# Kernel tuning notes

Hardware: AMD Instinct MI355X
Metric: run time of the kernel (lower is better)

## Reference

```python
import jax, jax.numpy as jnp
import numpy as np

STEP_SIZE = 0.01
ITERATION = 1.0
F_FORCING = 8.0
N_STEPS = int(round(ITERATION / STEP_SIZE))  # 100 fixed RK4 steps

BATCH = 8192
INPUT_SIZE = 784
SYSTEM_COUNT = 1024
OUTPUT_SIZE = 10


def setup_inputs() -> dict:
    key = jax.random.key(0)
    k_x, k_w1, k_b1, k_w2, k_b2 = jax.random.split(key, 5)
    x = jax.random.normal(k_x, (BATCH, INPUT_SIZE), dtype=jnp.float32)
    # nn.Linear-style params (out_features, in_features)
    s1 = 1.0 / np.sqrt(INPUT_SIZE)
    W1 = jax.random.uniform(k_w1, (SYSTEM_COUNT, INPUT_SIZE), jnp.float32, -s1, s1)
    b1 = jax.random.uniform(k_b1, (SYSTEM_COUNT,), jnp.float32, -s1, s1)
    s2 = 1.0 / np.sqrt(SYSTEM_COUNT)
    W2 = jax.random.uniform(k_w2, (OUTPUT_SIZE, SYSTEM_COUNT), jnp.float32, -s2, s2)
    b2 = jax.random.uniform(k_b2, (OUTPUT_SIZE,), jnp.float32, -s2, s2)
    return {"x": x, "W1": W1, "b1": b1, "W2": W2, "b2": b2}


def _lorenz96(x):
    # (roll(x,-1) - roll(x,2)) * roll(x,1) - x + F   along feature dim 1
    return (jnp.roll(x, -1, axis=1) - jnp.roll(x, 2, axis=1)) * jnp.roll(x, 1, axis=1) - x + F_FORCING


def _rk4_integrate(x0):
    h = jnp.float32(STEP_SIZE)

    def step(x, _):
        k1 = _lorenz96(x)
        k2 = _lorenz96(x + 0.5 * h * k1)
        k3 = _lorenz96(x + 0.5 * h * k2)
        k4 = _lorenz96(x + h * k3)
        x_next = x + (h / 6.0) * (k1 + 2.0 * k2 + 2.0 * k3 + k4)
        return x_next, None

    xT, _ = jax.lax.scan(step, x0, None, length=N_STEPS)
    return xT


def reference(x, W1, b1, W2, b2):
    h = x @ W1.T + b1                 # [B, systemCount]
    h = _rk4_integrate(h)             # RK4 over [0, iteration], step 0.01
    logits = h @ W2.T + b2            # [B, output_size]
    return jax.nn.log_softmax(logits, axis=1)
```

## Files before the change

kernel.cpp:

```cpp
#include <hip/hip_runtime.h>
#include <hip/hip_bf16.h>
#include <math.h>

#define BATCH 8192
#define INSZ 784
#define SYS 1024
#define OUTSZ 10
#define NSTEP 100
#define HSTEP 0.01f
#define FFORCE 8.0f

typedef short short8 __attribute__((ext_vector_type(8)));
typedef float float4v __attribute__((ext_vector_type(4)));
typedef float v2f __attribute__((ext_vector_type(2)));

static __device__ __forceinline__ short f2bf(float x) {
    __hip_bfloat16 b = __float2bfloat16(x);
    return __builtin_bit_cast(short, b);
}
static __device__ __forceinline__ float bf2f(short s) {
    unsigned int u = ((unsigned int)(unsigned short)s) << 16;
    return __builtin_bit_cast(float, u);
}

static __device__ __forceinline__ v2f pkfma(v2f a, v2f b, v2f c) {
    return __builtin_elementwise_fma(a, b, c);
}
static __device__ __forceinline__ v2f mk2(float x, float y) {
    v2f r; r.x = x; r.y = y; return r;
}
static __device__ __forceinline__ v2f sh2(v2f v, int ln) {
    v2f r; r.x = __shfl(v.x, ln); r.y = __shfl(v.y, ln); return r;
}

#define BM2 64
#define BN2 64
#define BK2 32
#define LDK2 40

__global__ __launch_bounds__(256, 4) void gemm1_kernel(
    const float* __restrict__ x, const float* __restrict__ W1,
    const float* __restrict__ b1, float* __restrict__ h)
{
    __shared__ short Ah[BM2 * LDK2], Al[BM2 * LDK2];
    __shared__ short Bh[BN2 * LDK2], Bl[BN2 * LDK2];

    const int t  = threadIdx.x;
    const int bm = blockIdx.y * BM2;
    const int bn = blockIdx.x * BN2;

    const int srow = t >> 2;
    const int kq   = (t & 3) * 8;

    const int wv   = t >> 6;
    const int lane = t & 63;
    const int lm   = lane & 15;
    const int q    = lane >> 4;

    float4v acc[4];
    #pragma unroll
    for (int j = 0; j < 4; ++j) {
        acc[j][0] = 0.f; acc[j][1] = 0.f; acc[j][2] = 0.f; acc[j][3] = 0.f;
    }

    const float* xa0 = x  + (size_t)(bm + srow) * INSZ + kq;
    const float* wb0 = W1 + (size_t)(bn + srow) * INSZ + kq;

    for (int it = 0; it < 25; ++it) {
        const int k0 = it * BK2;
        {
            const bool valid = (k0 + kq) < INSZ;
            float va[8], vb[8];
            if (valid) {
                #pragma unroll
                for (int p = 0; p < 2; ++p) {
                    float4 xv = ((const float4*)(xa0 + k0))[p];
                    float4 bv = ((const float4*)(wb0 + k0))[p];
                    va[4*p+0] = xv.x; va[4*p+1] = xv.y; va[4*p+2] = xv.z; va[4*p+3] = xv.w;
                    vb[4*p+0] = bv.x; vb[4*p+1] = bv.y; vb[4*p+2] = bv.z; vb[4*p+3] = bv.w;
                }
            } else {
                #pragma unroll
                for (int j = 0; j < 8; ++j) { va[j] = 0.f; vb[j] = 0.f; }
            }
            short8 ahi, alo, bhi, blo;
            #pragma unroll
            for (int j = 0; j < 8; ++j) {
                short h1 = f2bf(va[j]);
                short l1 = f2bf(va[j] - bf2f(h1));
                short h2 = f2bf(vb[j]);
                short l2 = f2bf(vb[j] - bf2f(h2));
                ahi[j] = h1;  alo[j] = l1;
                bhi[j] = h2;  blo[j] = l2;
            }
            const int base = srow * LDK2 + kq;
            *(short8*)&Ah[base] = ahi;
            *(short8*)&Al[base] = alo;
            *(short8*)&Bh[base] = bhi;
            *(short8*)&Bl[base] = blo;
        }
        __syncthreads();

        const int aoff = (wv * 16 + lm) * LDK2 + q * 8;
        short8 ah = *(const short8*)&Ah[aoff];
        short8 al = *(const short8*)&Al[aoff];
        #pragma unroll
        for (int fj = 0; fj < 4; ++fj) {
            const int boff = (fj * 16 + lm) * LDK2 + q * 8;
            short8 bh = *(const short8*)&Bh[boff];
            short8 bl = *(const short8*)&Bl[boff];
            acc[fj] = __builtin_amdgcn_mfma_f32_16x16x32_bf16(ah, bh, acc[fj], 0, 0, 0);
            acc[fj] = __builtin_amdgcn_mfma_f32_16x16x32_bf16(ah, bl, acc[fj], 0, 0, 0);
            acc[fj] = __builtin_amdgcn_mfma_f32_16x16x32_bf16(al, bh, acc[fj], 0, 0, 0);
        }
        __syncthreads();
    }

    #pragma unroll
    for (int fj = 0; fj < 4; ++fj) {
        const int col  = bn + fj * 16 + lm;
        const float bias = b1[col];
        const int row0 = bm + wv * 16 + q * 4;
        #pragma unroll
        for (int r = 0; r < 4; ++r)
            h[(size_t)(row0 + r) * SYS + col] = acc[fj][r] + bias;
    }
}

__global__ __launch_bounds__(256, 4) void rk4_kernel(
    const float* __restrict__ hbuf, const float* __restrict__ W2,
    const float* __restrict__ b2, float* __restrict__ out)
{
    const int lane = threadIdx.x & 63;
    const int w    = threadIdx.x >> 6;
    const int rowA = blockIdx.x * 8 + w * 2;
    const int rowB = rowA + 1;

    const int laneL = (lane + 63) & 63;
    const int laneR = (lane + 1) & 63;

    v2f X[16];
    {
        const float4* a4 = (const float4*)(hbuf + (size_t)rowA * SYS) + lane * 4;
        const float4* b4 = (const float4*)(hbuf + (size_t)rowB * SYS) + lane * 4;
        #pragma unroll
        for (int k = 0; k < 4; ++k) {
            float4 av = a4[k], bv = b4[k];
            X[4*k+0] = mk2(av.x, bv.x);
            X[4*k+1] = mk2(av.y, bv.y);
            X[4*k+2] = mk2(av.z, bv.z);
            X[4*k+3] = mk2(av.w, bv.w);
        }
    }

    const v2f Fv     = mk2(FFORCE, FFORCE);
    const v2f c_half = mk2(0.5f * HSTEP, 0.5f * HSTEP);
    const v2f c_full = mk2(HSTEP, HSTEP);
    const v2f c_two  = mk2(2.0f, 2.0f);
    const v2f c_six  = mk2(HSTEP / 6.0f, HSTEP / 6.0f);

    v2f acc[16], T[16];

    auto deriv_ip = [&](v2f (&y)[16], v2f r1, v2f l1, v2f l2) {
        v2f y0o = y[0], y1o = y[1], y2o = y[2];
        v2f d0 = Fv - y[0], d1 = Fv - y[1], d15 = Fv - y[15];
        v2f p2 = y0o, p1 = y1o, cur = y[2];
        #pragma unroll
        for (int i = 2; i < 15; ++i) {
            v2f yp1 = (i < 14) ? y[i + 1] : y[15];
            v2f nv  = pkfma(yp1 - p2, p1, Fv - cur);
            p2 = p1; p1 = cur;
            if (i < 14) cur = y[i + 1];
            y[i] = nv;
        }
        y[15] = pkfma(r1 - p2, p1, d15);
        y[1]  = pkfma(y2o - l1, y0o, d1);
        y[0]  = pkfma(y1o - l2, l1, d0);
    };

    v2f r1x = sh2(X[0],  laneR);
    v2f l1x = sh2(X[15], laneL);
    v2f l2x = sh2(X[14], laneL);

    #pragma unroll 1
    for (int s = 0; s < NSTEP; ++s) {
        #pragma unroll
        for (int i = 2; i < 15; ++i)
            acc[i] = pkfma(X[i + 1] - X[i - 2], X[i - 1], Fv - X[i]);
        acc[15] = pkfma(r1x - X[13], X[14], Fv - X[15]);
        acc[1]  = pkfma(X[2] - l1x, X[0],  Fv - X[1]);
        acc[0]  = pkfma(X[1] - l2x, l1x,   Fv - X[0]);

        T[14] = pkfma(c_half, acc[14], X[14]);
        T[15] = pkfma(c_half, acc[15], X[15]);
        T[0]  = pkfma(c_half, acc[0],  X[0]);
        v2f r1 = sh2(T[0],  laneR);
        v2f l1 = sh2(T[15], laneL);
        v2f l2 = sh2(T[14], laneL);
        #pragma unroll
        for (int i = 1; i < 14; ++i) T[i] = pkfma(c_half, acc[i], X[i]);
        deriv_ip(T, r1, l1, l2);

        {
            v2f a;
            a = T[14]; acc[14] = pkfma(c_two, a, acc[14]); T[14] = pkfma(c_half, a, X[14]);
            a = T[15]; acc[15] = pkfma(c_two, a, acc[15]); T[15] = pkfma(c_half, a, X[15]);
            a = T[0];  acc[0]  = pkfma(c_two, a, acc[0]);  T[0]  = pkfma(c_half, a, X[0]);
            r1 = sh2(T[0],  laneR);
            l1 = sh2(T[15], laneL);
            l2 = sh2(T[14], laneL);
            #pragma unroll
            for (int i = 1; i < 14; ++i) {
                a = T[i]; acc[i] = pkfma(c_two, a, acc[i]); T[i] = pkfma(c_half, a, X[i]);
            }
        }
        deriv_ip(T, r1, l1, l2);

        {
            v2f a;
            a = T[14]; acc[14] = pkfma(c_two, a, acc[14]); T[14] = pkfma(c_full, a, X[14]);
            a = T[15]; acc[15] = pkfma(c_two, a, acc[15]); T[15] = pkfma(c_full, a, X[15]);
            a = T[0];  acc[0]  = pkfma(c_two, a, acc[0]);  T[0]  = pkfma(c_full, a, X[0]);
            r1 = sh2(T[0],  laneR);
            l1 = sh2(T[15], laneL);
            l2 = sh2(T[14], laneL);
            #pragma unroll
            for (int i = 1; i < 14; ++i) {
                a = T[i]; acc[i] = pkfma(c_two, a, acc[i]); T[i] = pkfma(c_full, a, X[i]);
            }
        }
        deriv_ip(T, r1, l1, l2);

        X[14] = pkfma(c_six, acc[14] + T[14], X[14]);
        X[15] = pkfma(c_six, acc[15] + T[15], X[15]);
        X[0]  = pkfma(c_six, acc[0]  + T[0],  X[0]);
        r1x = sh2(X[0],  laneR);
        l1x = sh2(X[15], laneL);
        l2x = sh2(X[14], laneL);
        #pragma unroll
        for (int i = 1; i < 14; ++i)
            X[i] = pkfma(c_six, acc[i] + T[i], X[i]);
    }

    v2f l[OUTSZ];
    #pragma unroll
    for (int o = 0; o < OUTSZ; ++o) {
        const float4* w4 = (const float4*)(W2 + (size_t)o * SYS) + lane * 4;
        v2f s2 = mk2(0.f, 0.f);
        #pragma unroll
        for (int k = 0; k < 4; ++k) {
            float4 wv = w4[k];
            s2 = pkfma(X[4*k+0], mk2(wv.x, wv.x), s2);
            s2 = pkfma(X[4*k+1], mk2(wv.y, wv.y), s2);
            s2 = pkfma(X[4*k+2], mk2(wv.z, wv.z), s2);
            s2 = pkfma(X[4*k+3], mk2(wv.w, wv.w), s2);
        }
        #pragma unroll
        for (int dlt = 1; dlt < 64; dlt <<= 1) {
            s2.x += __shfl_xor(s2.x, dlt);
            s2.y += __shfl_xor(s2.y, dlt);
        }
        const float bo = b2[o];
        l[o] = s2 + mk2(bo, bo);
    }

    v2f m = l[0];
    #pragma unroll
    for (int o = 1; o < OUTSZ; ++o) m = __builtin_elementwise_max(m, l[o]);
    v2f ssum = mk2(0.f, 0.f);
    #pragma unroll
    for (int o = 0; o < OUTSZ; ++o) {
        v2f d = l[o] - m;
        ssum = ssum + mk2(__expf(d.x), __expf(d.y));
    }
    const v2f lse = m + mk2(__logf(ssum.x), __logf(ssum.y));

    float vA = l[0].x - lse.x;
    float vB = l[0].y - lse.y;
    #pragma unroll
    for (int o = 1; o < OUTSZ; ++o) {
        if (lane == o) { vA = l[o].x - lse.x; vB = l[o].y - lse.y; }
    }
    if (lane < OUTSZ) {
        out[(size_t)rowA * OUTSZ + lane] = vA;
        out[(size_t)rowB * OUTSZ + lane] = vB;
    }
}

extern "C" void kernel_launch(void* const* d_in, const int* in_sizes, int n_in,
                              void* d_out, int out_size, void* d_ws, size_t ws_size,
                              hipStream_t stream)
{
    const float* x  = (const float*)d_in[0];
    const float* W1 = (const float*)d_in[1];
    const float* b1 = (const float*)d_in[2];
    const float* W2 = (const float*)d_in[3];
    const float* b2 = (const float*)d_in[4];
    float* out = (float*)d_out;
    float* h   = (float*)d_ws;

    dim3 g1(SYS / BN2, BATCH / BM2);
    gemm1_kernel<<<g1, 256, 0, stream>>>(x, W1, b1, h);

    rk4_kernel<<<BATCH / 8, 256, 0, stream>>>(h, W2, b2, out);
}
```

Baseline: 416.6 us.

## Pre-split x and W1 into bf16 hi/lo buffers before GEMM1

Adds a conversion kernel that splits x and W1 once into padded bf16 high and low parts stored in workspace. A new GEMM kernel then loads the pre-split shorts directly instead of converting fp32 to bf16 pairs inside every tile, which removes the repeated conversions from the inner loop. The split buffers add an extra launch plus write and read traffic. The new path only runs when the workspace is large enough, otherwise the old kernel is used.

After: 430.0 us. 1.03x slower.

```diff
diff --git a/kernel.cpp b/kernel.cpp
--- a/kernel.cpp
+++ b/kernel.cpp
@@ -9,6 +9,7 @@
 #define NSTEP 100
 #define HSTEP 0.01f
 #define FFORCE 8.0f
+#define KP 800
 
 typedef short short8 __attribute__((ext_vector_type(8)));
 typedef float float4v __attribute__((ext_vector_type(4)));
@@ -31,12 +32,150 @@
 }
 static __device__ __forceinline__ v2f sh2(v2f v, int ln) {
     v2f r; r.x = __shfl(v.x, ln); r.y = __shfl(v.y, ln); return r;
+}
+
+__global__ __launch_bounds__(256) void convert_kernel(
+    const float* __restrict__ x, const float* __restrict__ W1,
+    short* __restrict__ xh, short* __restrict__ xl,
+    short* __restrict__ wh, short* __restrict__ wl)
+{
+    const int total = (BATCH + SYS) * (KP / 8);
+    for (int idx = blockIdx.x * blockDim.x + threadIdx.x; idx < total;
+         idx += gridDim.x * blockDim.x) {
+        const int row = idx / (KP / 8);
+        const int ck  = idx - row * (KP / 8);
+
+        short8 hi, lo;
+        if (ck < INSZ / 8) {
+            const float* src = (row < BATCH)
+                ? (x + (size_t)row * INSZ)
+                : (W1 + (size_t)(row - BATCH) * INSZ);
+            float4 v0 = ((const float4*)src)[ck * 2];
+            float4 v1 = ((const float4*)src)[ck * 2 + 1];
+            float vv[8] = {v0.x, v0.y, v0.z, v0.w, v1.x, v1.y, v1.z, v1.w};
+            #pragma unroll
+            for (int j = 0; j < 8; ++j) {
+                short hj = f2bf(vv[j]);
+                hi[j] = hj;
+                lo[j] = f2bf(vv[j] - bf2f(hj));
+            }
+        } else {
+            #pragma unroll
+            for (int j = 0; j < 8; ++j) { hi[j] = 0; lo[j] = 0; }
+        }
+
+        short* dh; short* dl;
+        if (row < BATCH) {
+            dh = xh + (size_t)row * KP;
+            dl = xl + (size_t)row * KP;
+        } else {
+            dh = wh + (size_t)(row - BATCH) * KP;
+            dl = wl + (size_t)(row - BATCH) * KP;
+        }
+        *(short8*)(dh + ck * 8) = hi;
+        *(short8*)(dl + ck * 8) = lo;
+    }
 }
 
 #define BM2 64
 #define BN2 64
 #define BK2 32
 #define LDK2 40
+
+__global__ __launch_bounds__(256, 4) void gemm1s_kernel(
+    const short* __restrict__ xh, const short* __restrict__ xl,
+    const short* __restrict__ wh, const short* __restrict__ wl,
+    const float* __restrict__ b1, float* __restrict__ h)
+{
+    __shared__ short Ah[BM2 * LDK2], Al[BM2 * LDK2];
+    __shared__ short Bh[BN2 * LDK2], Bl[BN2 * LDK2];
+
+    const int t  = threadIdx.x;
+    const int bm = blockIdx.y * BM2;
+    const int bn = blockIdx.x * BN2;
+
+    const int srow = t >> 2;
+    const int kq   = (t & 3) * 8;
+
+    const int wv   = t >> 6;
+    const int wr   = wv >> 1;
+    const int wc   = wv & 1;
+    const int lane = t & 63;
+    const int lm   = lane & 15;
+    const int q    = lane >> 4;
+
+    float4v acc[2][2];
+    #pragma unroll
+    for (int mi = 0; mi < 2; ++mi)
+        #pragma unroll
+        for (int nj = 0; nj < 2; ++nj) {
+            acc[mi][nj][0] = 0.f; acc[mi][nj][1] = 0.f;
+            acc[mi][nj][2] = 0.f; acc[mi][nj][3] = 0.f;
+        }
+
+    const short* pxh = xh + (size_t)(bm + srow) * KP + kq;
+    const short* pxl = xl + (size_t)(bm + srow) * KP + kq;
+    const short* pwh = wh + (size_t)(bn + srow) * KP + kq;
+    const short* pwl = wl + (size_t)(bn + srow) * KP + kq;
+    const int sbase = srow * LDK2 + kq;
+
+    short8 ra = *(const short8*)(pxh);
+    short8 rb = *(const short8*)(pxl);
+    short8 rc = *(const short8*)(pwh);
+    short8 rd = *(const short8*)(pwl);
+
+    for (int it = 0; it < 25; ++it) {
+        *(short8*)&Ah[sbase] = ra;
+        *(short8*)&Al[sbase] = rb;
+        *(short8*)&Bh[sbase] = rc;
+        *(short8*)&Bl[sbase] = rd;
+        __syncthreads();
+
+        if (it < 24) {
+            const int k1 = (it + 1) * BK2;
+            ra = *(const short8*)(pxh + k1);
+            rb = *(const short8*)(pxl + k1);
+            rc = *(const short8*)(pwh + k1);
+            rd = *(const short8*)(pwl + k1);
+        }
+
+        short8 fah[2], fal[2], fbh[2], fbl[2];
+        #pragma unroll
+        for (int mi = 0; mi < 2; ++mi) {
+            const int ao = (wr * 32 + mi * 16 + lm) * LDK2 + q * 8;
+            fah[mi] = *(const short8*)&Ah[ao];
+            fal[mi] = *(const short8*)&Al[ao];
+        }
+        #pragma unroll
+        for (int nj = 0; nj < 2; ++nj) {
+            const int bo = (wc * 32 + nj * 16 + lm) * LDK2 + q * 8;
+            fbh[nj] = *(const short8*)&Bh[bo];
+            fbl[nj] = *(const short8*)&Bl[bo];
+        }
+        #pragma unroll
+        for (int mi = 0; mi < 2; ++mi)
+            #pragma unroll
+            for (int nj = 0; nj < 2; ++nj) {
+                acc[mi][nj] = __builtin_amdgcn_mfma_f32_16x16x32_bf16(fah[mi], fbh[nj], acc[mi][nj], 0, 0, 0);
+                acc[mi][nj] = __builtin_amdgcn_mfma_f32_16x16x32_bf16(fah[mi], fbl[nj], acc[mi][nj], 0, 0, 0);
+                acc[mi][nj] = __builtin_amdgcn_mfma_f32_16x16x32_bf16(fal[mi], fbh[nj], acc[mi][nj], 0, 0, 0);
+            }
+        __syncthreads();
+    }
+
+    #pragma unroll
+    for (int mi = 0; mi < 2; ++mi) {
+        const int row0 = bm + wr * 32 + mi * 16 + q * 4;
+        #pragma unroll
+        for (int nj = 0; nj < 2; ++nj) {
+            const int col  = bn + wc * 32 + nj * 16 + lm;
+            const float bias = b1[col];
+            #pragma unroll
+            for (int r = 0; r < 4; ++r)
+                h[(size_t)(row0 + r) * SYS + col] = acc[mi][nj][r] + bias;
+        }
+    }
+}
 
 __global__ __launch_bounds__(256, 4) void gemm1_kernel(
     const float* __restrict__ x, const float* __restrict__ W1,
@@ -299,8 +438,22 @@
     float* out = (float*)d_out;
     float* h   = (float*)d_ws;
 
+    const size_t hbytes    = (size_t)BATCH * SYS * sizeof(float);
+    const size_t splitshorts = (size_t)(BATCH + SYS) * KP;
+    const size_t need      = hbytes + 2 * splitshorts * sizeof(short);
+
     dim3 g1(SYS / BN2, BATCH / BM2);
-    gemm1_kernel<<<g1, 256, 0, stream>>>(x, W1, b1, h);
+
+    if (ws_size >= need) {
+        short* xh = (short*)((char*)d_ws + hbytes);
+        short* xl = xh + (size_t)BATCH * KP;
+        short* wh = xl + (size_t)BATCH * KP;
+        short* wl = wh + (size_t)SYS * KP;
+        convert_kernel<<<2048, 256, 0, stream>>>(x, W1, xh, xl, wh, wl);
+        gemm1s_kernel<<<g1, 256, 0, stream>>>(xh, xl, wh, wl, b1, h);
+    } else {
+        gemm1_kernel<<<g1, 256, 0, stream>>>(x, W1, b1, h);
+    }
 
     rk4_kernel<<<BATCH / 8, 256, 0, stream>>>(h, W2, b2, out);
 }
```
